# Kernel optimization log

Measured on AMD Instinct MI355X. Metric: run time of the kernel, lower is better.

The kernel has to match this reference:

```python
import jax, jax.numpy as jnp
import numpy as np

DIM = 64  # QK head dim, matches init kwarg 'dim'

def setup_inputs() -> dict:
    key = jax.random.key(0)
    kq, kk, kv = jax.random.split(key, 3)
    B, L, C, D, H = 2, 2048, 16, DIM, 64
    query = jax.random.normal(kq, (B, L, C, D), dtype=jnp.float32)
    k_ = jax.random.normal(kk, (B, L, C, D), dtype=jnp.float32)
    value = jax.random.normal(kv, (B, L, C, H), dtype=jnp.float32)
    return {"query": query, "key": k_, "value": value}

def reference(query, key, value):
    scaler = 1.0 / jnp.sqrt(jnp.float32(DIM))
    # score: [b, c, l, m]
    score = jnp.einsum('blcd,bmcd->bclm', query, key) * scaler
    # mask=False, dropout=0 -> identity
    attn = jax.nn.softmax(score, axis=3)
    # out: [b, l, c, h]
    out = jnp.einsum('bmch,bclm->blch', value, attn)
    return out
```

## Files before the change

kernel.cpp:

```cpp
#include <hip/hip_runtime.h>
#include <hip/hip_bf16.h>
#include <stdint.h>

#define B_ 2
#define L_ 2048
#define C_ 16
#define D_ 64
#define H_ 64
#define QBLK 128
#define KVBLK 64
#define NTILES 32
#define NTHREADS 256
#define NHEADS 32
#define TILE_ELEMS 4096
#define TENSOR_ELEMS (NHEADS * NTILES * TILE_ELEMS)

typedef __attribute__((ext_vector_type(8))) short bf16x8;
typedef __attribute__((ext_vector_type(16))) float f32x16;
typedef __attribute__((ext_vector_type(8))) unsigned short u16x8;

__device__ inline unsigned short f2bf(float f) {
  union { float f; unsigned int u; } v; v.f = f;
  unsigned int u = v.u;
  unsigned int r = (u + 0x7FFFu + ((u >> 16) & 1u)) >> 16;
  return (unsigned short)r;
}

__device__ inline float fast_exp2(float x) {
#if __has_builtin(__builtin_amdgcn_exp2f)
  return __builtin_amdgcn_exp2f(x);
#else
  return exp2f(x);
#endif
}

__device__ inline void gload_lds16(const unsigned short* g, unsigned short* l) {
  __builtin_amdgcn_global_load_lds(
      (const __attribute__((address_space(1))) unsigned int*)g,
      (__attribute__((address_space(3))) unsigned int*)l, 16, 0, 0);
}

__device__ inline unsigned cvt_pk_bf16(float lo, float hi) {
  unsigned r;
  asm("v_cvt_pk_bf16_f32 %0, %1, %2" : "=v"(r) : "v"(lo), "v"(hi));
  return r;
}

__device__ inline void pl32swap(unsigned &x, unsigned &y) {
#if __has_builtin(__builtin_amdgcn_permlane32_swap)
  auto r = __builtin_amdgcn_permlane32_swap(x, y, false, false);
  x = r[0]; y = r[1];
#else
  asm("v_permlane32_swap_b32 %0, %1" : "+v"(x), "+&v"(y));
#endif
}

__device__ inline float xmax32(float v) {
  unsigned x = __float_as_uint(v), y = x;
  pl32swap(x, y);
  return fmaxf(__uint_as_float(x), __uint_as_float(y));
}

__device__ inline float xsum32(float v) {
  unsigned x = __float_as_uint(v), y = x;
  pl32swap(x, y);
  return __uint_as_float(x) + __uint_as_float(y);
}

__global__ __launch_bounds__(256) void prepack_kernel(
    const float* __restrict__ Kg, const float* __restrict__ Vg,
    unsigned short* __restrict__ Kb, unsigned short* __restrict__ Vb) {
  int idx = blockIdx.x * 256 + threadIdx.x;
  if (idx < 524288) {
    int i = idx;
    int grp = i & 7, row = (i >> 3) & 63, t = (i >> 9) & 31, head = i >> 14;
    int b = head >> 4, c = head & 15;
    const float* src = Kg + ((size_t)(b * L_ + t * 64 + row) * C_ + c) * D_ + grp * 8;
    float4 a0 = ((const float4*)src)[0];
    float4 a1 = ((const float4*)src)[1];
    u16x8 pk;
    pk[0] = f2bf(a0.x); pk[1] = f2bf(a0.y); pk[2] = f2bf(a0.z); pk[3] = f2bf(a0.w);
    pk[4] = f2bf(a1.x); pk[5] = f2bf(a1.y); pk[6] = f2bf(a1.z); pk[7] = f2bf(a1.w);
    size_t dst = ((size_t)(head * 32 + t) * 64 + row) * 64 + ((grp ^ (row & 7)) * 8);
    *(u16x8*)&Kb[dst] = pk;
  } else {
    int i = idx - 524288;
    int h = i & 63, grp = (i >> 6) & 7, t = (i >> 9) & 31, head = i >> 14;
    int b = head >> 4, c = head & 15;
    const float* src = Vg + ((size_t)(b * L_ + t * 64 + grp * 8) * C_ + c) * H_ + h;
    u16x8 pv;
#pragma unroll
    for (int j = 0; j < 8; ++j) pv[j] = f2bf(src[(size_t)j * C_ * H_]);
    size_t dst = ((size_t)(head * 32 + t) * 64 + h) * 64 + ((grp ^ (h & 7)) * 8);
    *(u16x8*)&Vb[dst] = pv;
  }
}

__global__ __launch_bounds__(NTHREADS, 2) void attn_fwd_kernel(
    const float* __restrict__ Qg,
    const unsigned short* __restrict__ Kb,
    const unsigned short* __restrict__ Vb,
    float* __restrict__ Og) {
  __shared__ unsigned short Ks2[2][TILE_ELEMS];
  __shared__ unsigned short Vt2[2][TILE_ELEMS];

  const int tid  = threadIdx.x;
  const int lane = tid & 63;
  const int w    = tid >> 6;
  const int ql   = lane & 31;
  const int u    = lane >> 5;

  const int bid   = blockIdx.x;
  const int swz   = (bid & 7) * 64 + (bid >> 3);
  const int head  = swz >> 4;
  const int qtile = swz & 15;
  const int b     = head >> 4;
  const int c     = head & 15;
  const int q0    = qtile * QBLK;

  const unsigned short* KbH = Kb + (size_t)head * NTILES * TILE_ELEMS;
  const unsigned short* VbH = Vb + (size_t)head * NTILES * TILE_ELEMS;

  const int qr = q0 + w * 32 + ql;
  const float* qrow = Qg + ((size_t)(b * L_ + qr) * C_ + c) * D_;
  bf16x8 qf[4];
#pragma unroll
  for (int ks = 0; ks < 4; ++ks) {
    float4 a0 = *(const float4*)(qrow + ks * 16 + u * 8);
    float4 a1 = *(const float4*)(qrow + ks * 16 + u * 8 + 4);
    bf16x8 q8;
    q8[0] = (short)f2bf(a0.x); q8[1] = (short)f2bf(a0.y);
    q8[2] = (short)f2bf(a0.z); q8[3] = (short)f2bf(a0.w);
    q8[4] = (short)f2bf(a1.x); q8[5] = (short)f2bf(a1.y);
    q8[6] = (short)f2bf(a1.z); q8[7] = (short)f2bf(a1.w);
    qf[ks] = q8;
  }

  f32x16 o0, o1;
#pragma unroll
  for (int i = 0; i < 16; ++i) { o0[i] = 0.f; o1[i] = 0.f; }
  float m_i = -1e30f, l_i = 0.f;
  const float sc2 = 0.125f * 1.44269504088896340736f;

  gload_lds16(KbH + tid * 8, &Ks2[0][tid * 8]);
  gload_lds16(KbH + 2048 + tid * 8, &Ks2[0][2048 + tid * 8]);
  gload_lds16(VbH + tid * 8, &Vt2[0][tid * 8]);
  gload_lds16(VbH + 2048 + tid * 8, &Vt2[0][2048 + tid * 8]);
  __syncthreads();

  int cur = 0;
  for (int t = 0; t < NTILES; ++t) {
    const unsigned short* KsB = Ks2[cur];
    const unsigned short* VtB = Vt2[cur];

    f32x16 s0, s1;
#pragma unroll
    for (int i = 0; i < 16; ++i) { s0[i] = 0.f; s1[i] = 0.f; }
#pragma unroll
    for (int ks = 0; ks < 4; ++ks) {
      const int col8 = 2 * ks + u;
      const int sw = (col8 ^ (ql & 7)) * 8;
      const bf16x8 ka0 = *(const bf16x8*)&KsB[ql * 64 + sw];
      const bf16x8 ka1 = *(const bf16x8*)&KsB[(32 + ql) * 64 + sw];
      s0 = __builtin_amdgcn_mfma_f32_32x32x16_bf16(ka0, qf[ks], s0, 0, 0, 0);
      s1 = __builtin_amdgcn_mfma_f32_32x32x16_bf16(ka1, qf[ks], s1, 0, 0, 0);
    }

    float rm = s0[0];
#pragma unroll
    for (int i = 1; i < 16; ++i) rm = fmaxf(rm, s0[i]);
#pragma unroll
    for (int i = 0; i < 16; ++i) rm = fmaxf(rm, s1[i]);
    rm = xmax32(rm);
    const float rmx = rm * sc2;
    if (__any(rmx > m_i + 8.f)) {
      float mn = fmaxf(m_i, rmx);
      float so = fast_exp2(m_i - mn);
      m_i = mn;
#pragma unroll
      for (int i = 0; i < 16; ++i) { o0[i] *= so; o1[i] *= so; }
      l_i *= so;
    }

    float rs = 0.f;
    bf16x8 pf[4];
#pragma unroll
    for (int tq = 0; tq < 4; ++tq) {
      const int be = ((2 * tq) & 3) * 4;
      const int bo = ((2 * tq + 1) & 3) * 4;
      float p0[4], p1[4];
#pragma unroll
      for (int r = 0; r < 4; ++r) {
        float se = (tq < 2) ? s0[be + r] : s1[be + r];
        float so_ = (tq < 2) ? s0[bo + r] : s1[bo + r];
        p0[r] = fast_exp2(__builtin_fmaf(se, sc2, -m_i));
        p1[r] = fast_exp2(__builtin_fmaf(so_, sc2, -m_i));
        rs += p0[r] + p1[r];
      }
      unsigned x0 = cvt_pk_bf16(p0[0], p0[1]);
      unsigned x1 = cvt_pk_bf16(p0[2], p0[3]);
      unsigned y0 = cvt_pk_bf16(p1[0], p1[1]);
      unsigned y1 = cvt_pk_bf16(p1[2], p1[3]);
      pl32swap(x0, y0);
      pl32swap(x1, y1);
      union { unsigned wd[4]; bf16x8 v; } pk;
      pk.wd[0] = x0; pk.wd[1] = x1; pk.wd[2] = y0; pk.wd[3] = y1;
      pf[tq] = pk.v;
    }
    l_i += xsum32(rs);

    if (t + 1 < NTILES) {
      const size_t toff = (size_t)(t + 1) * TILE_ELEMS + tid * 8;
      const int nb = cur ^ 1;
      gload_lds16(KbH + toff, &Ks2[nb][tid * 8]);
      gload_lds16(KbH + toff + 2048, &Ks2[nb][2048 + tid * 8]);
      gload_lds16(VbH + toff, &Vt2[nb][tid * 8]);
      gload_lds16(VbH + toff + 2048, &Vt2[nb][2048 + tid * 8]);
    }

#pragma unroll
    for (int m = 0; m < 4; ++m) {
      const int col8 = 2 * m + u;
      const int sw = (col8 ^ (ql & 7)) * 8;
      const bf16x8 va0 = *(const bf16x8*)&VtB[ql * 64 + sw];
      const bf16x8 va1 = *(const bf16x8*)&VtB[(32 + ql) * 64 + sw];
      o0 = __builtin_amdgcn_mfma_f32_32x32x16_bf16(va0, pf[m], o0, 0, 0, 0);
      o1 = __builtin_amdgcn_mfma_f32_32x32x16_bf16(va1, pf[m], o1, 0, 0, 0);
    }

    __syncthreads();
    cur ^= 1;
  }

  const float inv = 1.0f / l_i;
  float* orow = Og + ((size_t)(b * L_ + qr) * C_ + c) * H_;
#pragma unroll
  for (int rg = 0; rg < 4; ++rg) {
    float4 v0, v1;
    v0.x = o0[rg * 4 + 0] * inv; v0.y = o0[rg * 4 + 1] * inv;
    v0.z = o0[rg * 4 + 2] * inv; v0.w = o0[rg * 4 + 3] * inv;
    v1.x = o1[rg * 4 + 0] * inv; v1.y = o1[rg * 4 + 1] * inv;
    v1.z = o1[rg * 4 + 2] * inv; v1.w = o1[rg * 4 + 3] * inv;
    *(float4*)(orow + 8 * rg + 4 * u) = v0;
    *(float4*)(orow + 32 + 8 * rg + 4 * u) = v1;
  }
}

extern "C" void kernel_launch(void* const* d_in, const int* in_sizes, int n_in,
                              void* d_out, int out_size, void* d_ws, size_t ws_size,
                              hipStream_t stream) {
  const float* Qg = (const float*)d_in[0];
  const float* Kg = (const float*)d_in[1];
  const float* Vg = (const float*)d_in[2];
  float* Og = (float*)d_out;

  unsigned short* Kb = (unsigned short*)d_ws;
  unsigned short* Vb = Kb + (size_t)TENSOR_ELEMS;

  prepack_kernel<<<4096, 256, 0, stream>>>(Kg, Vg, Kb, Vb);

  dim3 grid(NHEADS * (L_ / QBLK));
  dim3 block(NTHREADS);
  attn_fwd_kernel<<<grid, block, 0, stream>>>(Qg, Kb, Vb, Og);
}
```

Baseline: 65.52 us.

## Triple-buffer K/V tiles with explicit vmcnt waits, setprio, and wider LDS swizzle

Moves from double to triple buffering of the K/V LDS tiles and issues the load for tile t+2 at the start of each iteration. The blanket __syncthreads is replaced by an explicit vmcnt(4) wait plus s_barrier, so there is more time for global-to-LDS loads to land. It also extends the XOR swizzle with bit 3 of the row to cut LDS bank conflicts, raises wave priority around the MFMA blocks, and turns the max and sum reductions into trees. The cost is 48KB of LDS per block, which may limit how many blocks fit per CU, plus redundant loads of the last tile near the end of the loop.

New measurement: 69.04 us. 5.4% more time.

```diff
diff --git a/kernel.cpp b/kernel.cpp
--- a/kernel.cpp
+++ b/kernel.cpp
@@ -66,6 +66,8 @@
   pl32swap(x, y);
   return __uint_as_float(x) + __uint_as_float(y);
 }
+
+#define SLOT(grp, row) ((grp) ^ ((row) & 7) ^ (((row) & 8) >> 1))
 
 __global__ __launch_bounds__(256) void prepack_kernel(
     const float* __restrict__ Kg, const float* __restrict__ Vg,
@@ -81,7 +83,7 @@
     u16x8 pk;
     pk[0] = f2bf(a0.x); pk[1] = f2bf(a0.y); pk[2] = f2bf(a0.z); pk[3] = f2bf(a0.w);
     pk[4] = f2bf(a1.x); pk[5] = f2bf(a1.y); pk[6] = f2bf(a1.z); pk[7] = f2bf(a1.w);
-    size_t dst = ((size_t)(head * 32 + t) * 64 + row) * 64 + ((grp ^ (row & 7)) * 8);
+    size_t dst = ((size_t)(head * 32 + t) * 64 + row) * 64 + SLOT(grp, row) * 8;
     *(u16x8*)&Kb[dst] = pk;
   } else {
     int i = idx - 524288;
@@ -91,7 +93,7 @@
     u16x8 pv;
 #pragma unroll
     for (int j = 0; j < 8; ++j) pv[j] = f2bf(src[(size_t)j * C_ * H_]);
-    size_t dst = ((size_t)(head * 32 + t) * 64 + h) * 64 + ((grp ^ (h & 7)) * 8);
+    size_t dst = ((size_t)(head * 32 + t) * 64 + h) * 64 + SLOT(grp, h) * 8;
     *(u16x8*)&Vb[dst] = pv;
   }
 }
@@ -101,8 +103,8 @@
     const unsigned short* __restrict__ Kb,
     const unsigned short* __restrict__ Vb,
     float* __restrict__ Og) {
-  __shared__ unsigned short Ks2[2][TILE_ELEMS];
-  __shared__ unsigned short Vt2[2][TILE_ELEMS];
+  __shared__ unsigned short Ks2[3][TILE_ELEMS];
+  __shared__ unsigned short Vt2[3][TILE_ELEMS];
 
   const int tid  = threadIdx.x;
   const int lane = tid & 63;
@@ -146,31 +148,50 @@
   gload_lds16(KbH + 2048 + tid * 8, &Ks2[0][2048 + tid * 8]);
   gload_lds16(VbH + tid * 8, &Vt2[0][tid * 8]);
   gload_lds16(VbH + 2048 + tid * 8, &Vt2[0][2048 + tid * 8]);
-  __syncthreads();
-
-  int cur = 0;
+  gload_lds16(KbH + TILE_ELEMS + tid * 8, &Ks2[1][tid * 8]);
+  gload_lds16(KbH + TILE_ELEMS + 2048 + tid * 8, &Ks2[1][2048 + tid * 8]);
+  gload_lds16(VbH + TILE_ELEMS + tid * 8, &Vt2[1][tid * 8]);
+  gload_lds16(VbH + TILE_ELEMS + 2048 + tid * 8, &Vt2[1][2048 + tid * 8]);
+  asm volatile("s_waitcnt vmcnt(4)" ::: "memory");
+  __builtin_amdgcn_s_barrier();
+  __builtin_amdgcn_sched_barrier(0);
+
+  int cur = 0, stg = 2;
   for (int t = 0; t < NTILES; ++t) {
+    {
+      const int tl = (t + 2 < NTILES) ? (t + 2) : (NTILES - 1);
+      const size_t toff = (size_t)tl * TILE_ELEMS + tid * 8;
+      gload_lds16(KbH + toff, &Ks2[stg][tid * 8]);
+      gload_lds16(KbH + toff + 2048, &Ks2[stg][2048 + tid * 8]);
+      gload_lds16(VbH + toff, &Vt2[stg][tid * 8]);
+      gload_lds16(VbH + toff + 2048, &Vt2[stg][2048 + tid * 8]);
+    }
+
     const unsigned short* KsB = Ks2[cur];
     const unsigned short* VtB = Vt2[cur];
 
     f32x16 s0, s1;
 #pragma unroll
     for (int i = 0; i < 16; ++i) { s0[i] = 0.f; s1[i] = 0.f; }
+    __builtin_amdgcn_s_setprio(1);
 #pragma unroll
     for (int ks = 0; ks < 4; ++ks) {
       const int col8 = 2 * ks + u;
-      const int sw = (col8 ^ (ql & 7)) * 8;
+      const int sw = SLOT(col8, ql) * 8;
       const bf16x8 ka0 = *(const bf16x8*)&KsB[ql * 64 + sw];
       const bf16x8 ka1 = *(const bf16x8*)&KsB[(32 + ql) * 64 + sw];
       s0 = __builtin_amdgcn_mfma_f32_32x32x16_bf16(ka0, qf[ks], s0, 0, 0, 0);
       s1 = __builtin_amdgcn_mfma_f32_32x32x16_bf16(ka1, qf[ks], s1, 0, 0, 0);
     }
-
-    float rm = s0[0];
-#pragma unroll
-    for (int i = 1; i < 16; ++i) rm = fmaxf(rm, s0[i]);
-#pragma unroll
-    for (int i = 0; i < 16; ++i) rm = fmaxf(rm, s1[i]);
+    __builtin_amdgcn_s_setprio(0);
+
+    float a8[8];
+#pragma unroll
+    for (int i = 0; i < 8; ++i)
+      a8[i] = fmaxf(fmaxf(s0[i], s0[i + 8]), fmaxf(s1[i], s1[i + 8]));
+    float b4a = fmaxf(a8[0], a8[1]), b4b = fmaxf(a8[2], a8[3]);
+    float b4c = fmaxf(a8[4], a8[5]), b4d = fmaxf(a8[6], a8[7]);
+    float rm = fmaxf(fmaxf(b4a, b4b), fmaxf(b4c, b4d));
     rm = xmax32(rm);
     const float rmx = rm * sc2;
     if (__any(rmx > m_i + 8.f)) {
@@ -182,7 +203,7 @@
       l_i *= so;
     }
 
-    float rs = 0.f;
+    float rst[4];
     bf16x8 pf[4];
 #pragma unroll
     for (int tq = 0; tq < 4; ++tq) {
@@ -195,8 +216,9 @@
         float so_ = (tq < 2) ? s0[bo + r] : s1[bo + r];
         p0[r] = fast_exp2(__builtin_fmaf(se, sc2, -m_i));
         p1[r] = fast_exp2(__builtin_fmaf(so_, sc2, -m_i));
-        rs += p0[r] + p1[r];
       }
+      rst[tq] = ((p0[0] + p0[1]) + (p0[2] + p0[3])) +
+                ((p1[0] + p1[1]) + (p1[2] + p1[3]));
       unsigned x0 = cvt_pk_bf16(p0[0], p0[1]);
       unsigned x1 = cvt_pk_bf16(p0[2], p0[3]);
       unsigned y0 = cvt_pk_bf16(p1[0], p1[1]);
@@ -207,29 +229,27 @@
       pk.wd[0] = x0; pk.wd[1] = x1; pk.wd[2] = y0; pk.wd[3] = y1;
       pf[tq] = pk.v;
     }
-    l_i += xsum32(rs);
-
-    if (t + 1 < NTILES) {
-      const size_t toff = (size_t)(t + 1) * TILE_ELEMS + tid * 8;
-      const int nb = cur ^ 1;
-      gload_lds16(KbH + toff, &Ks2[nb][tid * 8]);
-      gload_lds16(KbH + toff + 2048, &Ks2[nb][2048 + tid * 8]);
-      gload_lds16(VbH + toff, &Vt2[nb][tid * 8]);
-      gload_lds16(VbH + toff + 2048, &Vt2[nb][2048 + tid * 8]);
-    }
-
+    l_i += xsum32((rst[0] + rst[1]) + (rst[2] + rst[3]));
+
+    __builtin_amdgcn_s_setprio(1);
 #pragma unroll
     for (int m = 0; m < 4; ++m) {
       const int col8 = 2 * m + u;
-      const int sw = (col8 ^ (ql & 7)) * 8;
+      const int sw = SLOT(col8, ql) * 8;
       const bf16x8 va0 = *(const bf16x8*)&VtB[ql * 64 + sw];
       const bf16x8 va1 = *(const bf16x8*)&VtB[(32 + ql) * 64 + sw];
       o0 = __builtin_amdgcn_mfma_f32_32x32x16_bf16(va0, pf[m], o0, 0, 0, 0);
       o1 = __builtin_amdgcn_mfma_f32_32x32x16_bf16(va1, pf[m], o1, 0, 0, 0);
     }
-
-    __syncthreads();
-    cur ^= 1;
+    __builtin_amdgcn_s_setprio(0);
+
+    __builtin_amdgcn_sched_barrier(0);
+    asm volatile("s_waitcnt vmcnt(4) lgkmcnt(0)" ::: "memory");
+    __builtin_amdgcn_s_barrier();
+    __builtin_amdgcn_sched_barrier(0);
+
+    cur = (cur == 2) ? 0 : cur + 1;
+    stg = (stg == 2) ? 0 : stg + 1;
   }
 
   const float inv = 1.0f / l_i;
```
